# Optimization experiments

Measured on AMD Instinct MI355X. Metric: run time of the kernel, lower is better.

The kernel has to match this reference:

```python
import jax, jax.numpy as jnp
import numpy as np

B, T, D_IN, H = 256, 512, 64, 128
S_MIN, S_FRAC = 0.5, 0.5


def _gru_cell(x_i, h, W_ih, W_hh, b_ih, b_hh):
    # torch.nn.GRUCell semantics
    gi = x_i @ W_ih.T + b_ih          # [B, 3H]
    gh = h @ W_hh.T + b_hh            # [B, 3H]
    i_r, i_z, i_n = jnp.split(gi, 3, axis=-1)
    h_r, h_z, h_n = jnp.split(gh, 3, axis=-1)
    r = jax.nn.sigmoid(i_r + h_r)
    z = jax.nn.sigmoid(i_z + h_z)
    n = jnp.tanh(i_n + r * h_n)
    return (1.0 - z) * n + z * h


def _rk4_step(h, dt, W_node, b_node):
    # one fixed RK4 step of dh/dt = tanh(h @ W_node^T + b_node) over [t, t+dt]
    f = lambda hh: jnp.tanh(hh @ W_node.T + b_node)
    k1 = f(h)
    k2 = f(h + 0.5 * dt * k1)
    k3 = f(h + 0.5 * dt * k2)
    k4 = f(h + dt * k3)
    return h + (dt / 6.0) * (k1 + 2.0 * k2 + 2.0 * k3 + k4)


def setup_inputs() -> dict:
    key = jax.random.key(0)
    ks = jax.random.split(key, 8)
    x = jax.random.normal(ks[0], (B, T, D_IN), dtype=jnp.float32)
    # sorted per-sample time grid; all lens == T so argmax-longest picks row 0
    tp = jnp.broadcast_to(jnp.linspace(0.01, 1.0, T, dtype=jnp.float32), (B, T))
    # generate_samp_mask(x, s_min=0.5, s_frac=0.5), deterministic seed
    rng = np.random.default_rng(0)
    minimum_ind = int(T * S_MIN)
    extrap_ind = int(rng.integers(minimum_ind, T))
    n_inds = int(S_FRAC * extrap_ind)
    samp_inds = np.sort(rng.choice(np.arange(extrap_ind), n_inds, replace=False))
    mask_np = np.zeros(T, dtype=bool)
    mask_np[samp_inds] = True
    samp_mask = jnp.asarray(mask_np)
    s = 1.0 / np.sqrt(H)
    W_ih = jax.random.uniform(ks[1], (3 * H, D_IN), jnp.float32, -s, s)
    W_hh = jax.random.uniform(ks[2], (3 * H, H), jnp.float32, -s, s)
    b_ih = jax.random.uniform(ks[3], (3 * H,), jnp.float32, -s, s)
    b_hh = jax.random.uniform(ks[4], (3 * H,), jnp.float32, -s, s)
    W_node = jax.random.normal(ks[5], (H, H), jnp.float32) * 0.05
    b_node = jnp.zeros((H,), jnp.float32)
    W_out = jax.random.uniform(ks[6], (D_IN, H), jnp.float32, -s, s)
    b_out = jax.random.uniform(ks[7], (D_IN,), jnp.float32, -s, s)
    return {"x": x, "tp": tp, "samp_mask": samp_mask,
            "W_ih": W_ih, "W_hh": W_hh, "b_ih": b_ih, "b_hh": b_hh,
            "W_node": W_node, "b_node": b_node, "W_out": W_out, "b_out": b_out}


def reference(x, tp, samp_mask, W_ih, W_hh, b_ih, b_hh, W_node, b_node, W_out, b_out):
    # get_longest_tp: all lens equal -> row 0; prepend tp[0]-0.01
    t0 = tp[0]                                   # [T]
    ts = jnp.concatenate([t0[:1] - 0.01, t0])    # [T+1]
    dts = ts[1:] - ts[:-1]                       # [T]
    xs = jnp.transpose(x, (1, 0, 2))             # [T, B, D_in]
    h0 = jnp.zeros((x.shape[0], W_hh.shape[1]), x.dtype)

    def step(h, inp):
        dt, x_i, use_x = inp
        h_ode = _rk4_step(h, dt, W_node, b_node)
        prev_out = h @ W_out.T + b_out           # teacher-forcing from own output
        inp_vec = jnp.where(use_x, x_i, prev_out)
        h_new = _gru_cell(inp_vec, h_ode, W_ih, W_hh, b_ih, b_hh)
        return h_new, h_new

    _, h_arr = jax.lax.scan(step, h0, (dts, xs, samp_mask))  # [T, B, H]
    h_arr = jnp.transpose(h_arr, (1, 0, 2))                  # [B, T, H]
    out = h_arr @ W_out.T + b_out                            # [B, T, D_in]
    # select_by_length with all lens == T -> flat [B*T, D_in]
    return out.reshape(-1, out.shape[-1])
```

## Files before the change

### kernel.cpp

```cpp
#include <hip/hip_runtime.h>


#define NB    256
#define TB    512
#define TSTEP 512
#define DIN   64
#define HD    128

typedef float v2f __attribute__((ext_vector_type(2)));

__device__ __forceinline__ float fast_tanh(float v) {
    float e = __expf(2.0f * v);
    return 1.0f - 2.0f / (e + 1.0f);
}
__device__ __forceinline__ float fast_sigmoid(float v) {
    return 1.0f / (1.0f + __expf(-v));
}

__device__ __forceinline__ void sync_lds() {
    asm volatile("s_waitcnt lgkmcnt(0)" ::: "memory");
    __builtin_amdgcn_s_barrier();
    asm volatile("" ::: "memory");
}

template<int PAT>
__device__ __forceinline__ float dpp_xadd(float v) {
    return v + __int_as_float(__builtin_amdgcn_update_dpp(
        0, __float_as_int(v), PAT, 0xF, 0xF, true));
}
template<int OFF>
__device__ __forceinline__ float swz(float v) {
    return __int_as_float(__builtin_amdgcn_ds_swizzle(__float_as_int(v), OFF));
}
__device__ __forceinline__ float red8(float v) {
    v = dpp_xadd<0xB1>(v);
    v = dpp_xadd<0x4E>(v);
    return v + swz<0x101F>(v);
}
__device__ __forceinline__ float red8_split(float pA, float pB, bool low) {
    pA = dpp_xadd<0xB1>(pA);  pB = dpp_xadd<0xB1>(pB);
    pA = dpp_xadd<0x4E>(pA);  pB = dpp_xadd<0x4E>(pB);
    float keep = low ? pA : pB;
    float send = low ? pB : pA;
    return keep + swz<0x101F>(send);
}

__global__ __launch_bounds__(TB, 2) void gruode_kernel(
    const float* __restrict__ x,
    const float* __restrict__ tp,
    const int*   __restrict__ samp_mask,
    const float* __restrict__ W_ih,
    const float* __restrict__ W_hh,
    const float* __restrict__ b_ih,
    const float* __restrict__ b_hh,
    const float* __restrict__ W_node,
    const float* __restrict__ b_node,
    const float* __restrict__ W_out,
    const float* __restrict__ b_out,
    float*       __restrict__ out)
{
    const int t    = threadIdx.x;
    const int b    = blockIdx.x;
    const int jp   = t >> 3;
    const int ks   = t & 7;
    const bool low = (ks & 4) == 0;
    const int jm   = 2 * jp + (ks >> 2);
    const bool own = (ks & 3) == 0;

    __shared__ __align__(16) float sh_h [HD];
    __shared__ __align__(16) float sh_t0[HD];
    __shared__ __align__(16) float sh_t1[HD];
    __shared__ __align__(16) float sh_in[DIN];
    __shared__ __align__(16) float sh_po[DIN];
    __shared__ float sh_dt[TSTEP];
    __shared__ int   sh_mk[TSTEP];

    const float4* Wn4  = (const float4*)W_node;
    const float4* Whh4 = (const float4*)W_hh;
    const float4* Wih4 = (const float4*)W_ih;
    const float4* Wo4  = (const float4*)W_out;

    v2f WnA[8], WnB[8], WhrA[8], WhrB[8], WhzA[8], WhzB[8], WhnA[8], WhnB[8];
    #pragma unroll
    for (int ii = 0; ii < 4; ++ii) {
        float4 w;
        const int c = ii * 8 + ks;
        w = Wn4 [(2*jp  )*32 + c];        WnA [2*ii] = (v2f){w.x,w.y}; WnA [2*ii+1] = (v2f){w.z,w.w};
        w = Wn4 [(2*jp+1)*32 + c];        WnB [2*ii] = (v2f){w.x,w.y}; WnB [2*ii+1] = (v2f){w.z,w.w};
        w = Whh4[(0*HD + 2*jp  )*32 + c]; WhrA[2*ii] = (v2f){w.x,w.y}; WhrA[2*ii+1] = (v2f){w.z,w.w};
        w = Whh4[(0*HD + 2*jp+1)*32 + c]; WhrB[2*ii] = (v2f){w.x,w.y}; WhrB[2*ii+1] = (v2f){w.z,w.w};
        w = Whh4[(1*HD + 2*jp  )*32 + c]; WhzA[2*ii] = (v2f){w.x,w.y}; WhzA[2*ii+1] = (v2f){w.z,w.w};
        w = Whh4[(1*HD + 2*jp+1)*32 + c]; WhzB[2*ii] = (v2f){w.x,w.y}; WhzB[2*ii+1] = (v2f){w.z,w.w};
        w = Whh4[(2*HD + 2*jp  )*32 + c]; WhnA[2*ii] = (v2f){w.x,w.y}; WhnA[2*ii+1] = (v2f){w.z,w.w};
        w = Whh4[(2*HD + 2*jp+1)*32 + c]; WhnB[2*ii] = (v2f){w.x,w.y}; WhnB[2*ii+1] = (v2f){w.z,w.w};
    }
    v2f WirA[4], WirB[4], WizA[4], WizB[4], WinA[4], WinB[4], Wo[8];
    #pragma unroll
    for (int ii = 0; ii < 2; ++ii) {
        float4 w;
        const int c = ii * 8 + ks;
        w = Wih4[(0*HD + 2*jp  )*16 + c]; WirA[2*ii] = (v2f){w.x,w.y}; WirA[2*ii+1] = (v2f){w.z,w.w};
        w = Wih4[(0*HD + 2*jp+1)*16 + c]; WirB[2*ii] = (v2f){w.x,w.y}; WirB[2*ii+1] = (v2f){w.z,w.w};
        w = Wih4[(1*HD + 2*jp  )*16 + c]; WizA[2*ii] = (v2f){w.x,w.y}; WizA[2*ii+1] = (v2f){w.z,w.w};
        w = Wih4[(1*HD + 2*jp+1)*16 + c]; WizB[2*ii] = (v2f){w.x,w.y}; WizB[2*ii+1] = (v2f){w.z,w.w};
        w = Wih4[(2*HD + 2*jp  )*16 + c]; WinA[2*ii] = (v2f){w.x,w.y}; WinA[2*ii+1] = (v2f){w.z,w.w};
        w = Wih4[(2*HD + 2*jp+1)*16 + c]; WinB[2*ii] = (v2f){w.x,w.y}; WinB[2*ii+1] = (v2f){w.z,w.w};
    }
    #pragma unroll
    for (int ii = 0; ii < 4; ++ii) {
        float4 w = Wo4[jp*32 + ii*8 + ks];
        Wo[2*ii] = (v2f){w.x,w.y}; Wo[2*ii+1] = (v2f){w.z,w.w};
    }
    #pragma unroll
    for (int ii = 0; ii < 8; ++ii) {
        asm volatile("" : "+v"(WnA[ii]));  asm volatile("" : "+v"(WnB[ii]));
        asm volatile("" : "+v"(WhrA[ii])); asm volatile("" : "+v"(WhrB[ii]));
        asm volatile("" : "+v"(WhzA[ii])); asm volatile("" : "+v"(WhzB[ii]));
        asm volatile("" : "+v"(WhnA[ii])); asm volatile("" : "+v"(WhnB[ii]));
        asm volatile("" : "+v"(Wo[ii]));
    }
    #pragma unroll
    for (int ii = 0; ii < 4; ++ii) {
        asm volatile("" : "+v"(WirA[ii])); asm volatile("" : "+v"(WirB[ii]));
        asm volatile("" : "+v"(WizA[ii])); asm volatile("" : "+v"(WizB[ii]));
        asm volatile("" : "+v"(WinA[ii])); asm volatile("" : "+v"(WinB[ii]));
    }

    const float bn_s = b_node[jm];
    const float br_s = b_ih[0*HD + jm] + b_hh[0*HD + jm];
    const float bz_s = b_ih[1*HD + jm] + b_hh[1*HD + jm];
    const float bi_s = b_ih[2*HD + jm];
    const float bh_s = b_hh[2*HD + jm];
    const float bo   = b_out[jp];

    if (t < HD) sh_h[t] = 0.0f;
    {
        float tc = tp[t];
        float tq = (t == 0) ? tc - 0.01f : tp[t - 1];
        sh_dt[t] = tc - tq;
        sh_mk[t] = samp_mask[t];
    }

    const float* xbase = x   + (size_t)b * TSTEP * DIN;
    float*       obase = out + (size_t)b * TSTEP * DIN;
    float xr = (t < DIN) ? xbase[t] : 0.0f;

    sync_lds();

    const float4* h4  = (const float4*)sh_h;
    const float4* t04 = (const float4*)sh_t0;
    const float4* t14 = (const float4*)sh_t1;
    const float4* in4 = (const float4*)sh_in;

    auto dot2 = [&](const v2f (&wA)[8], const v2f (&wB)[8], const float4* buf,
                    float& rA, float& rB) {
        v2f aA = {0.f,0.f}, bA = {0.f,0.f}, aB = {0.f,0.f}, bB = {0.f,0.f};
        #pragma unroll
        for (int ii = 0; ii < 4; ++ii) {
            float4 v = buf[ii*8 + ks];
            v2f lo = {v.x, v.y}, hi = {v.z, v.w};
            aA += wA[2*ii] * lo;  bA += wA[2*ii+1] * hi;
            aB += wB[2*ii] * lo;  bB += wB[2*ii+1] * hi;
        }
        v2f sA = aA + bA, sB = aB + bB;
        rA = sA.x + sA.y;  rB = sB.x + sB.y;
    };

    float hj = 0.0f;

    #pragma unroll 1
    for (int s = 0; s < TSTEP; ++s) {
        const float dt = sh_dt[s];
        const int   mc = sh_mk[s];
        float k1, k2, k3;

        {
            float4 v0 = h4[ks], v1 = h4[8+ks], v2 = h4[16+ks], v3 = h4[24+ks];
            v2f l0 = {v0.x,v0.y}, u0 = {v0.z,v0.w};
            v2f l1 = {v1.x,v1.y}, u1 = {v1.z,v1.w};
            v2f l2 = {v2.x,v2.y}, u2 = {v2.z,v2.w};
            v2f l3 = {v3.x,v3.y}, u3 = {v3.z,v3.w};
            v2f aA = WnA[0]*l0 + WnA[1]*u0 + WnA[2]*l1 + WnA[3]*u1
                   + WnA[4]*l2 + WnA[5]*u2 + WnA[6]*l3 + WnA[7]*u3;
            v2f aB = WnB[0]*l0 + WnB[1]*u0 + WnB[2]*l1 + WnB[3]*u1
                   + WnB[4]*l2 + WnB[5]*u2 + WnB[6]*l3 + WnB[7]*u3;
            v2f ao = Wo[0]*l0 + Wo[1]*u0 + Wo[2]*l1 + Wo[3]*u1
                   + Wo[4]*l2 + Wo[5]*u2 + Wo[6]*l3 + Wo[7]*u3;
            k1 = fast_tanh(red8_split(aA.x + aA.y, aB.x + aB.y, low) + bn_s);
            float o = red8(ao.x + ao.y) + bo;
            if (ks == 0) {
                sh_po[jp] = o;
                if (s > 0) obase[(size_t)(s - 1) * DIN + jp] = o;
            }
            if (own) sh_t0[jm] = fmaf(0.5f * dt, k1, hj);
        }
        sync_lds();

        if (t < DIN) sh_in[t] = mc ? xr : sh_po[t];
        {
            float rA, rB;
            dot2(WnA, WnB, t04, rA, rB);
            k2 = fast_tanh(red8_split(rA, rB, low) + bn_s);
            if (own) sh_t1[jm] = fmaf(0.5f * dt, k2, hj);
        }
        {
            const int sn = (s + 1 < TSTEP) ? s + 1 : s;
            if (t < DIN) xr = xbase[(size_t)sn * DIN + t];
        }
        sync_lds();

        float crA, crB, czA, czB, cnA, cnB;
        {
            float rA, rB;
            dot2(WnA, WnB, t14, rA, rB);
            k3 = fast_tanh(red8_split(rA, rB, low) + bn_s);

            float4 v0 = in4[ks], v1 = in4[8 + ks];
            v2f lo0 = {v0.x,v0.y}, hi0 = {v0.z,v0.w};
            v2f lo1 = {v1.x,v1.y}, hi1 = {v1.z,v1.w};
            v2f cr0 = WirA[0]*lo0 + WirA[1]*hi0 + WirA[2]*lo1 + WirA[3]*hi1;
            v2f cr1 = WirB[0]*lo0 + WirB[1]*hi0 + WirB[2]*lo1 + WirB[3]*hi1;
            v2f cz0 = WizA[0]*lo0 + WizA[1]*hi0 + WizA[2]*lo1 + WizA[3]*hi1;
            v2f cz1 = WizB[0]*lo0 + WizB[1]*hi0 + WizB[2]*lo1 + WizB[3]*hi1;
            v2f cn0 = WinA[0]*lo0 + WinA[1]*hi0 + WinA[2]*lo1 + WinA[3]*hi1;
            v2f cn1 = WinB[0]*lo0 + WinB[1]*hi0 + WinB[2]*lo1 + WinB[3]*hi1;
            crA = cr0.x + cr0.y;  crB = cr1.x + cr1.y;
            czA = cz0.x + cz0.y;  czB = cz1.x + cz1.y;
            cnA = cn0.x + cn0.y;  cnB = cn1.x + cn1.y;

            if (own) sh_t0[jm] = fmaf(dt, k3, hj);
        }
        sync_lds();

        float hode = 0.0f;
        {
            float rA, rB;
            dot2(WnA, WnB, t04, rA, rB);
            float k4 = fast_tanh(red8_split(rA, rB, low) + bn_s);
            hode = fmaf(dt * (1.0f / 6.0f),
                        (k1 + 2.0f * k2) + (2.0f * k3 + k4), hj);
            if (own) sh_t1[jm] = hode;
        }
        sync_lds();

        {
            float4 v0 = t14[ks], v1 = t14[8+ks], v2 = t14[16+ks], v3 = t14[24+ks];
            v2f l0 = {v0.x,v0.y}, u0 = {v0.z,v0.w};
            v2f l1 = {v1.x,v1.y}, u1 = {v1.z,v1.w};
            v2f l2 = {v2.x,v2.y}, u2 = {v2.z,v2.w};
            v2f l3 = {v3.x,v3.y}, u3 = {v3.z,v3.w};
            v2f arA = WhrA[0]*l0 + WhrA[1]*u0 + WhrA[2]*l1 + WhrA[3]*u1
                    + WhrA[4]*l2 + WhrA[5]*u2 + WhrA[6]*l3 + WhrA[7]*u3;
            v2f arB = WhrB[0]*l0 + WhrB[1]*u0 + WhrB[2]*l1 + WhrB[3]*u1
                    + WhrB[4]*l2 + WhrB[5]*u2 + WhrB[6]*l3 + WhrB[7]*u3;
            v2f azA = WhzA[0]*l0 + WhzA[1]*u0 + WhzA[2]*l1 + WhzA[3]*u1
                    + WhzA[4]*l2 + WhzA[5]*u2 + WhzA[6]*l3 + WhzA[7]*u3;
            v2f azB = WhzB[0]*l0 + WhzB[1]*u0 + WhzB[2]*l1 + WhzB[3]*u1
                    + WhzB[4]*l2 + WhzB[5]*u2 + WhzB[6]*l3 + WhzB[7]*u3;
            v2f anA = WhnA[0]*l0 + WhnA[1]*u0 + WhnA[2]*l1 + WhnA[3]*u1
                    + WhnA[4]*l2 + WhnA[5]*u2 + WhnA[6]*l3 + WhnA[7]*u3;
            v2f anB = WhnB[0]*l0 + WhnB[1]*u0 + WhnB[2]*l1 + WhnB[3]*u1
                    + WhnB[4]*l2 + WhnB[5]*u2 + WhnB[6]*l3 + WhnB[7]*u3;

            float r_ = red8_split((arA.x + arA.y) + crA, (arB.x + arB.y) + crB, low);
            float z_ = red8_split((azA.x + azA.y) + czA, (azB.x + azB.y) + czB, low);
            float hn = red8_split(anA.x + anA.y, anB.x + anB.y, low);
            float in_ = red8_split(cnA, cnB, low);

            float rr = fast_sigmoid(r_ + br_s);
            float zz = fast_sigmoid(z_ + bz_s);
            float nn = fast_tanh(fmaf(rr, hn + bh_s, in_ + bi_s));
            float hnew = fmaf(zz, hode - nn, nn);
            hj = hnew;
            if (own) sh_h[jm] = hnew;
        }
        sync_lds();
    }

    {
        float4 v0 = h4[ks], v1 = h4[8+ks], v2 = h4[16+ks], v3 = h4[24+ks];
        v2f l0 = {v0.x,v0.y}, u0 = {v0.z,v0.w};
        v2f l1 = {v1.x,v1.y}, u1 = {v1.z,v1.w};
        v2f l2 = {v2.x,v2.y}, u2 = {v2.z,v2.w};
        v2f l3 = {v3.x,v3.y}, u3 = {v3.z,v3.w};
        v2f ao = Wo[0]*l0 + Wo[1]*u0 + Wo[2]*l1 + Wo[3]*u1
               + Wo[4]*l2 + Wo[5]*u2 + Wo[6]*l3 + Wo[7]*u3;
        float o = red8(ao.x + ao.y) + bo;
        if (ks == 0) obase[(size_t)(TSTEP - 1) * DIN + jp] = o;
    }
}

extern "C" void kernel_launch(void* const* d_in, const int* in_sizes, int n_in,
                              void* d_out, int out_size, void* d_ws, size_t ws_size,
                              hipStream_t stream) {
    (void)in_sizes; (void)n_in; (void)d_ws; (void)ws_size; (void)out_size;
    const float* x      = (const float*)d_in[0];
    const float* tp     = (const float*)d_in[1];
    const int*   mask   = (const int*)  d_in[2];
    const float* W_ih   = (const float*)d_in[3];
    const float* W_hh   = (const float*)d_in[4];
    const float* b_ih   = (const float*)d_in[5];
    const float* b_hh   = (const float*)d_in[6];
    const float* W_node = (const float*)d_in[7];
    const float* b_node = (const float*)d_in[8];
    const float* W_out  = (const float*)d_in[9];
    const float* b_out  = (const float*)d_in[10];
    float* outp = (float*)d_out;

    gruode_kernel<<<NB, TB, 0, stream>>>(x, tp, mask, W_ih, W_hh, b_ih, b_hh,
                                         W_node, b_node, W_out, b_out, outp);
}
```

Baseline: 1.099 ms.

## Remap threads to 16-lane groups of four rows with DPP row reductions

Threads are regrouped from 8 lanes covering two output rows into 16 lanes covering four rows, so each lane reads half as many float4 values from shared memory per matvec. The cross-lane reduction now uses only DPP moves (quad add, row_shr, row_bcast-style patterns) in place of ds_swizzle. This is meant to cut LDS read traffic and reduction latency on the serial per-step critical path. In exchange each lane holds four rows of weights, which changes the register layout, and it relies on the DPP patterns having correct semantics within 16-lane rows.

```diff
diff --git a/kernel.cpp b/kernel.cpp
--- a/kernel.cpp
+++ b/kernel.cpp
@@ -28,21 +28,37 @@
     return v + __int_as_float(__builtin_amdgcn_update_dpp(
         0, __float_as_int(v), PAT, 0xF, 0xF, true));
 }
-template<int OFF>
-__device__ __forceinline__ float swz(float v) {
-    return __int_as_float(__builtin_amdgcn_ds_swizzle(__float_as_int(v), OFF));
-}
-__device__ __forceinline__ float red8(float v) {
+template<int PAT>
+__device__ __forceinline__ float dpp_mov(float v) {
+    return __int_as_float(__builtin_amdgcn_update_dpp(
+        0, __float_as_int(v), PAT, 0xF, 0xF, true));
+}
+__device__ __forceinline__ float qred(float v) {
     v = dpp_xadd<0xB1>(v);
-    v = dpp_xadd<0x4E>(v);
-    return v + swz<0x101F>(v);
-}
-__device__ __forceinline__ float red8_split(float pA, float pB, bool low) {
-    pA = dpp_xadd<0xB1>(pA);  pB = dpp_xadd<0xB1>(pB);
-    pA = dpp_xadd<0x4E>(pA);  pB = dpp_xadd<0x4E>(pB);
-    float keep = low ? pA : pB;
-    float send = low ? pB : pA;
-    return keep + swz<0x101F>(send);
+    return dpp_xadd<0x4E>(v);
+}
+__device__ __forceinline__ float red16x4(float p0, float p1, float p2, float p3,
+                                         bool b2, bool b3) {
+    p0 = qred(p0); p1 = qred(p1); p2 = qred(p2); p3 = qred(p3);
+    float u  = b2 ? p2 : p0;
+    float us = b2 ? p0 : p2;
+    float v  = b2 ? p3 : p1;
+    float vs = b2 ? p1 : p3;
+    u += dpp_mov<0x141>(us);
+    v += dpp_mov<0x141>(vs);
+    float w  = b3 ? v : u;
+    float ws = b3 ? u : v;
+    w += dpp_mov<0x128>(ws);
+    return w;
+}
+__device__ __forceinline__ float red16x2(float p0, float p1, bool b3) {
+    p0 = qred(p0); p1 = qred(p1);
+    p0 += dpp_mov<0x141>(p0);
+    p1 += dpp_mov<0x141>(p1);
+    float w  = b3 ? p1 : p0;
+    float ws = b3 ? p0 : p1;
+    w += dpp_mov<0x128>(ws);
+    return w;
 }
 
 __global__ __launch_bounds__(TB, 2) void gruode_kernel(
@@ -61,11 +77,14 @@
 {
     const int t    = threadIdx.x;
     const int b    = blockIdx.x;
-    const int jp   = t >> 3;
-    const int ks   = t & 7;
-    const bool low = (ks & 4) == 0;
-    const int jm   = 2 * jp + (ks >> 2);
-    const bool own = (ks & 3) == 0;
+    const int g    = t >> 4;
+    const int ks2  = t & 15;
+    const bool b2  = (ks2 & 4)  != 0;
+    const bool b3  = (ks2 & 8)  != 0;
+    const int jm   = 4*g + (b2 ? 2 : 0) + (b3 ? 1 : 0);
+    const bool own = (ks2 & 3) == 0;
+    const int jo   = 2*g + (b3 ? 1 : 0);
+    const bool oown= (ks2 & 7) == 0;
 
     __shared__ __align__(16) float sh_h [HD];
     __shared__ __align__(16) float sh_t0[HD];
@@ -80,50 +99,47 @@
     const float4* Wih4 = (const float4*)W_ih;
     const float4* Wo4  = (const float4*)W_out;
 
-    v2f WnA[8], WnB[8], WhrA[8], WhrB[8], WhzA[8], WhzB[8], WhnA[8], WhnB[8];
-    #pragma unroll
-    for (int ii = 0; ii < 4; ++ii) {
-        float4 w;
-        const int c = ii * 8 + ks;
-        w = Wn4 [(2*jp  )*32 + c];        WnA [2*ii] = (v2f){w.x,w.y}; WnA [2*ii+1] = (v2f){w.z,w.w};
-        w = Wn4 [(2*jp+1)*32 + c];        WnB [2*ii] = (v2f){w.x,w.y}; WnB [2*ii+1] = (v2f){w.z,w.w};
-        w = Whh4[(0*HD + 2*jp  )*32 + c]; WhrA[2*ii] = (v2f){w.x,w.y}; WhrA[2*ii+1] = (v2f){w.z,w.w};
-        w = Whh4[(0*HD + 2*jp+1)*32 + c]; WhrB[2*ii] = (v2f){w.x,w.y}; WhrB[2*ii+1] = (v2f){w.z,w.w};
-        w = Whh4[(1*HD + 2*jp  )*32 + c]; WhzA[2*ii] = (v2f){w.x,w.y}; WhzA[2*ii+1] = (v2f){w.z,w.w};
-        w = Whh4[(1*HD + 2*jp+1)*32 + c]; WhzB[2*ii] = (v2f){w.x,w.y}; WhzB[2*ii+1] = (v2f){w.z,w.w};
-        w = Whh4[(2*HD + 2*jp  )*32 + c]; WhnA[2*ii] = (v2f){w.x,w.y}; WhnA[2*ii+1] = (v2f){w.z,w.w};
-        w = Whh4[(2*HD + 2*jp+1)*32 + c]; WhnB[2*ii] = (v2f){w.x,w.y}; WhnB[2*ii+1] = (v2f){w.z,w.w};
-    }
-    v2f WirA[4], WirB[4], WizA[4], WizB[4], WinA[4], WinB[4], Wo[8];
-    #pragma unroll
-    for (int ii = 0; ii < 2; ++ii) {
-        float4 w;
-        const int c = ii * 8 + ks;
-        w = Wih4[(0*HD + 2*jp  )*16 + c]; WirA[2*ii] = (v2f){w.x,w.y}; WirA[2*ii+1] = (v2f){w.z,w.w};
-        w = Wih4[(0*HD + 2*jp+1)*16 + c]; WirB[2*ii] = (v2f){w.x,w.y}; WirB[2*ii+1] = (v2f){w.z,w.w};
-        w = Wih4[(1*HD + 2*jp  )*16 + c]; WizA[2*ii] = (v2f){w.x,w.y}; WizA[2*ii+1] = (v2f){w.z,w.w};
-        w = Wih4[(1*HD + 2*jp+1)*16 + c]; WizB[2*ii] = (v2f){w.x,w.y}; WizB[2*ii+1] = (v2f){w.z,w.w};
-        w = Wih4[(2*HD + 2*jp  )*16 + c]; WinA[2*ii] = (v2f){w.x,w.y}; WinA[2*ii+1] = (v2f){w.z,w.w};
-        w = Wih4[(2*HD + 2*jp+1)*16 + c]; WinB[2*ii] = (v2f){w.x,w.y}; WinB[2*ii+1] = (v2f){w.z,w.w};
-    }
-    #pragma unroll
-    for (int ii = 0; ii < 4; ++ii) {
-        float4 w = Wo4[jp*32 + ii*8 + ks];
-        Wo[2*ii] = (v2f){w.x,w.y}; Wo[2*ii+1] = (v2f){w.z,w.w};
-    }
-    #pragma unroll
-    for (int ii = 0; ii < 8; ++ii) {
-        asm volatile("" : "+v"(WnA[ii]));  asm volatile("" : "+v"(WnB[ii]));
-        asm volatile("" : "+v"(WhrA[ii])); asm volatile("" : "+v"(WhrB[ii]));
-        asm volatile("" : "+v"(WhzA[ii])); asm volatile("" : "+v"(WhzB[ii]));
-        asm volatile("" : "+v"(WhnA[ii])); asm volatile("" : "+v"(WhnB[ii]));
-        asm volatile("" : "+v"(Wo[ii]));
-    }
-    #pragma unroll
-    for (int ii = 0; ii < 4; ++ii) {
-        asm volatile("" : "+v"(WirA[ii])); asm volatile("" : "+v"(WirB[ii]));
-        asm volatile("" : "+v"(WizA[ii])); asm volatile("" : "+v"(WizB[ii]));
-        asm volatile("" : "+v"(WinA[ii])); asm volatile("" : "+v"(WinB[ii]));
+    v2f Wn[16], Whr[16], Whz[16], Whn[16];
+    #pragma unroll
+    for (int r = 0; r < 4; ++r) {
+        const int row = 4*g + r;
+        float4 a, c;
+        a = Wn4 [row*32 + ks2];      Wn [4*r+0]=(v2f){a.x,a.y}; Wn [4*r+1]=(v2f){a.z,a.w};
+        c = Wn4 [row*32 + 16 + ks2]; Wn [4*r+2]=(v2f){c.x,c.y}; Wn [4*r+3]=(v2f){c.z,c.w};
+        a = Whh4[(0*HD+row)*32 + ks2];      Whr[4*r+0]=(v2f){a.x,a.y}; Whr[4*r+1]=(v2f){a.z,a.w};
+        c = Whh4[(0*HD+row)*32 + 16 + ks2]; Whr[4*r+2]=(v2f){c.x,c.y}; Whr[4*r+3]=(v2f){c.z,c.w};
+        a = Whh4[(1*HD+row)*32 + ks2];      Whz[4*r+0]=(v2f){a.x,a.y}; Whz[4*r+1]=(v2f){a.z,a.w};
+        c = Whh4[(1*HD+row)*32 + 16 + ks2]; Whz[4*r+2]=(v2f){c.x,c.y}; Whz[4*r+3]=(v2f){c.z,c.w};
+        a = Whh4[(2*HD+row)*32 + ks2];      Whn[4*r+0]=(v2f){a.x,a.y}; Whn[4*r+1]=(v2f){a.z,a.w};
+        c = Whh4[(2*HD+row)*32 + 16 + ks2]; Whn[4*r+2]=(v2f){c.x,c.y}; Whn[4*r+3]=(v2f){c.z,c.w};
+    }
+    v2f Wir[8], Wiz[8], Win[8];
+    #pragma unroll
+    for (int r = 0; r < 4; ++r) {
+        const int row = 4*g + r;
+        float4 a;
+        a = Wih4[(0*HD+row)*16 + ks2]; Wir[2*r]=(v2f){a.x,a.y}; Wir[2*r+1]=(v2f){a.z,a.w};
+        a = Wih4[(1*HD+row)*16 + ks2]; Wiz[2*r]=(v2f){a.x,a.y}; Wiz[2*r+1]=(v2f){a.z,a.w};
+        a = Wih4[(2*HD+row)*16 + ks2]; Win[2*r]=(v2f){a.x,a.y}; Win[2*r+1]=(v2f){a.z,a.w};
+    }
+    v2f Wo[8];
+    #pragma unroll
+    for (int o = 0; o < 2; ++o) {
+        const int row = 2*g + o;
+        float4 a = Wo4[row*32 + ks2];
+        float4 c = Wo4[row*32 + 16 + ks2];
+        Wo[4*o+0]=(v2f){a.x,a.y}; Wo[4*o+1]=(v2f){a.z,a.w};
+        Wo[4*o+2]=(v2f){c.x,c.y}; Wo[4*o+3]=(v2f){c.z,c.w};
+    }
+    #pragma unroll
+    for (int i = 0; i < 16; ++i) {
+        asm volatile("" : "+v"(Wn[i]));  asm volatile("" : "+v"(Whr[i]));
+        asm volatile("" : "+v"(Whz[i])); asm volatile("" : "+v"(Whn[i]));
+    }
+    #pragma unroll
+    for (int i = 0; i < 8; ++i) {
+        asm volatile("" : "+v"(Wir[i])); asm volatile("" : "+v"(Wiz[i]));
+        asm volatile("" : "+v"(Win[i])); asm volatile("" : "+v"(Wo[i]));
     }
 
     const float bn_s = b_node[jm];
@@ -131,7 +147,7 @@
     const float bz_s = b_ih[1*HD + jm] + b_hh[1*HD + jm];
     const float bi_s = b_ih[2*HD + jm];
     const float bh_s = b_hh[2*HD + jm];
-    const float bo   = b_out[jp];
+    const float bo_s = b_out[jo];
 
     if (t < HD) sh_h[t] = 0.0f;
     {
@@ -152,18 +168,18 @@
     const float4* t14 = (const float4*)sh_t1;
     const float4* in4 = (const float4*)sh_in;
 
-    auto dot2 = [&](const v2f (&wA)[8], const v2f (&wB)[8], const float4* buf,
-                    float& rA, float& rB) {
-        v2f aA = {0.f,0.f}, bA = {0.f,0.f}, aB = {0.f,0.f}, bB = {0.f,0.f};
+    auto lds2 = [&](const float4* buf, v2f& l0, v2f& u0, v2f& l1, v2f& u1) {
+        float4 v0 = buf[ks2], v1 = buf[16 + ks2];
+        l0 = (v2f){v0.x, v0.y}; u0 = (v2f){v0.z, v0.w};
+        l1 = (v2f){v1.x, v1.y}; u1 = (v2f){v1.z, v1.w};
+    };
+    auto dot4 = [&](const v2f (&W)[16], v2f l0, v2f u0, v2f l1, v2f u1,
+                    float (&p)[4]) {
         #pragma unroll
-        for (int ii = 0; ii < 4; ++ii) {
-            float4 v = buf[ii*8 + ks];
-            v2f lo = {v.x, v.y}, hi = {v.z, v.w};
-            aA += wA[2*ii] * lo;  bA += wA[2*ii+1] * hi;
-            aB += wB[2*ii] * lo;  bB += wB[2*ii+1] * hi;
-        }
-        v2f sA = aA + bA, sB = aB + bB;
-        rA = sA.x + sA.y;  rB = sB.x + sB.y;
+        for (int r = 0; r < 4; ++r) {
+            v2f a = W[4*r]*l0 + W[4*r+1]*u0 + W[4*r+2]*l1 + W[4*r+3]*u1;
+            p[r] = a.x + a.y;
+        }
     };
 
     float hj = 0.0f;
@@ -175,22 +191,15 @@
         float k1, k2, k3;
 
         {
-            float4 v0 = h4[ks], v1 = h4[8+ks], v2 = h4[16+ks], v3 = h4[24+ks];
-            v2f l0 = {v0.x,v0.y}, u0 = {v0.z,v0.w};
-            v2f l1 = {v1.x,v1.y}, u1 = {v1.z,v1.w};
-            v2f l2 = {v2.x,v2.y}, u2 = {v2.z,v2.w};
-            v2f l3 = {v3.x,v3.y}, u3 = {v3.z,v3.w};
-            v2f aA = WnA[0]*l0 + WnA[1]*u0 + WnA[2]*l1 + WnA[3]*u1
-                   + WnA[4]*l2 + WnA[5]*u2 + WnA[6]*l3 + WnA[7]*u3;
-            v2f aB = WnB[0]*l0 + WnB[1]*u0 + WnB[2]*l1 + WnB[3]*u1
-                   + WnB[4]*l2 + WnB[5]*u2 + WnB[6]*l3 + WnB[7]*u3;
-            v2f ao = Wo[0]*l0 + Wo[1]*u0 + Wo[2]*l1 + Wo[3]*u1
-                   + Wo[4]*l2 + Wo[5]*u2 + Wo[6]*l3 + Wo[7]*u3;
-            k1 = fast_tanh(red8_split(aA.x + aA.y, aB.x + aB.y, low) + bn_s);
-            float o = red8(ao.x + ao.y) + bo;
-            if (ks == 0) {
-                sh_po[jp] = o;
-                if (s > 0) obase[(size_t)(s - 1) * DIN + jp] = o;
+            v2f l0,u0,l1,u1; lds2(h4, l0,u0,l1,u1);
+            float p[4]; dot4(Wn, l0,u0,l1,u1, p);
+            v2f ao0 = Wo[0]*l0 + Wo[1]*u0 + Wo[2]*l1 + Wo[3]*u1;
+            v2f ao1 = Wo[4]*l0 + Wo[5]*u0 + Wo[6]*l1 + Wo[7]*u1;
+            k1 = fast_tanh(red16x4(p[0],p[1],p[2],p[3], b2,b3) + bn_s);
+            float o = red16x2(ao0.x + ao0.y, ao1.x + ao1.y, b3) + bo_s;
+            if (oown) {
+                sh_po[jo] = o;
+                if (s > 0) obase[(size_t)(s - 1) * DIN + jo] = o;
             }
             if (own) sh_t0[jm] = fmaf(0.5f * dt, k1, hj);
         }
@@ -198,9 +207,9 @@
 
         if (t < DIN) sh_in[t] = mc ? xr : sh_po[t];
         {
-            float rA, rB;
-            dot2(WnA, WnB, t04, rA, rB);
-            k2 = fast_tanh(red8_split(rA, rB, low) + bn_s);
+            v2f l0,u0,l1,u1; lds2(t04, l0,u0,l1,u1);
+            float p[4]; dot4(Wn, l0,u0,l1,u1, p);
+            k2 = fast_tanh(red16x4(p[0],p[1],p[2],p[3], b2,b3) + bn_s);
             if (own) sh_t1[jm] = fmaf(0.5f * dt, k2, hj);
         }
         {
@@ -209,34 +218,30 @@
         }
         sync_lds();
 
-        float crA, crB, czA, czB, cnA, cnB;
-        {
-            float rA, rB;
-            dot2(WnA, WnB, t14, rA, rB);
-            k3 = fast_tanh(red8_split(rA, rB, low) + bn_s);
-
-            float4 v0 = in4[ks], v1 = in4[8 + ks];
-            v2f lo0 = {v0.x,v0.y}, hi0 = {v0.z,v0.w};
-            v2f lo1 = {v1.x,v1.y}, hi1 = {v1.z,v1.w};
-            v2f cr0 = WirA[0]*lo0 + WirA[1]*hi0 + WirA[2]*lo1 + WirA[3]*hi1;
-            v2f cr1 = WirB[0]*lo0 + WirB[1]*hi0 + WirB[2]*lo1 + WirB[3]*hi1;
-            v2f cz0 = WizA[0]*lo0 + WizA[1]*hi0 + WizA[2]*lo1 + WizA[3]*hi1;
-            v2f cz1 = WizB[0]*lo0 + WizB[1]*hi0 + WizB[2]*lo1 + WizB[3]*hi1;
-            v2f cn0 = WinA[0]*lo0 + WinA[1]*hi0 + WinA[2]*lo1 + WinA[3]*hi1;
-            v2f cn1 = WinB[0]*lo0 + WinB[1]*hi0 + WinB[2]*lo1 + WinB[3]*hi1;
-            crA = cr0.x + cr0.y;  crB = cr1.x + cr1.y;
-            czA = cz0.x + cz0.y;  czB = cz1.x + cz1.y;
-            cnA = cn0.x + cn0.y;  cnB = cn1.x + cn1.y;
-
+        float cr[4], cz[4], cn[4];
+        {
+            v2f l0,u0,l1,u1; lds2(t14, l0,u0,l1,u1);
+            float p[4]; dot4(Wn, l0,u0,l1,u1, p);
+            k3 = fast_tanh(red16x4(p[0],p[1],p[2],p[3], b2,b3) + bn_s);
+
+            float4 vi = in4[ks2];
+            v2f li = (v2f){vi.x, vi.y}, ui = (v2f){vi.z, vi.w};
+            #pragma unroll
+            for (int r = 0; r < 4; ++r) {
+                v2f a = Wir[2*r]*li + Wir[2*r+1]*ui;
+                v2f c = Wiz[2*r]*li + Wiz[2*r+1]*ui;
+                v2f d = Win[2*r]*li + Win[2*r+1]*ui;
+                cr[r] = a.x + a.y;  cz[r] = c.x + c.y;  cn[r] = d.x + d.y;
+            }
             if (own) sh_t0[jm] = fmaf(dt, k3, hj);
         }
         sync_lds();
 
-        float hode = 0.0f;
-        {
-            float rA, rB;
-            dot2(WnA, WnB, t04, rA, rB);
-            float k4 = fast_tanh(red8_split(rA, rB, low) + bn_s);
+        float hode;
+        {
+            v2f l0,u0,l1,u1; lds2(t04, l0,u0,l1,u1);
+            float p[4]; dot4(Wn, l0,u0,l1,u1, p);
+            float k4 = fast_tanh(red16x4(p[0],p[1],p[2],p[3], b2,b3) + bn_s);
             hode = fmaf(dt * (1.0f / 6.0f),
                         (k1 + 2.0f * k2) + (2.0f * k3 + k4), hj);
             if (own) sh_t1[jm] = hode;
@@ -244,32 +249,19 @@
         sync_lds();
 
         {
-            float4 v0 = t14[ks], v1 = t14[8+ks], v2 = t14[16+ks], v3 = t14[24+ks];
-            v2f l0 = {v0.x,v0.y}, u0 = {v0.z,v0.w};
-            v2f l1 = {v1.x,v1.y}, u1 = {v1.z,v1.w};
-            v2f l2 = {v2.x,v2.y}, u2 = {v2.z,v2.w};
-            v2f l3 = {v3.x,v3.y}, u3 = {v3.z,v3.w};
-            v2f arA = WhrA[0]*l0 + WhrA[1]*u0 + WhrA[2]*l1 + WhrA[3]*u1
-                    + WhrA[4]*l2 + WhrA[5]*u2 + WhrA[6]*l3 + WhrA[7]*u3;
-            v2f arB = WhrB[0]*l0 + WhrB[1]*u0 + WhrB[2]*l1 + WhrB[3]*u1
-                    + WhrB[4]*l2 + WhrB[5]*u2 + WhrB[6]*l3 + WhrB[7]*u3;
-            v2f azA = WhzA[0]*l0 + WhzA[1]*u0 + WhzA[2]*l1 + WhzA[3]*u1
-                    + WhzA[4]*l2 + WhzA[5]*u2 + WhzA[6]*l3 + WhzA[7]*u3;
-            v2f azB = WhzB[0]*l0 + WhzB[1]*u0 + WhzB[2]*l1 + WhzB[3]*u1
-                    + WhzB[4]*l2 + WhzB[5]*u2 + WhzB[6]*l3 + WhzB[7]*u3;
-            v2f anA = WhnA[0]*l0 + WhnA[1]*u0 + WhnA[2]*l1 + WhnA[3]*u1
-                    + WhnA[4]*l2 + WhnA[5]*u2 + WhnA[6]*l3 + WhnA[7]*u3;
-            v2f anB = WhnB[0]*l0 + WhnB[1]*u0 + WhnB[2]*l1 + WhnB[3]*u1
-                    + WhnB[4]*l2 + WhnB[5]*u2 + WhnB[6]*l3 + WhnB[7]*u3;
-
-            float r_ = red8_split((arA.x + arA.y) + crA, (arB.x + arB.y) + crB, low);
-            float z_ = red8_split((azA.x + azA.y) + czA, (azB.x + azB.y) + czB, low);
-            float hn = red8_split(anA.x + anA.y, anB.x + anB.y, low);
-            float in_ = red8_split(cnA, cnB, low);
+            v2f l0,u0,l1,u1; lds2(t14, l0,u0,l1,u1);
+            float ar[4], az[4], an[4];
+            dot4(Whr, l0,u0,l1,u1, ar);
+            dot4(Whz, l0,u0,l1,u1, az);
+            dot4(Whn, l0,u0,l1,u1, an);
+            float r_  = red16x4(ar[0]+cr[0], ar[1]+cr[1], ar[2]+cr[2], ar[3]+cr[3], b2,b3);
+            float z_  = red16x4(az[0]+cz[0], az[1]+cz[1], az[2]+cz[2], az[3]+cz[3], b2,b3);
+            float hn  = red16x4(an[0], an[1], an[2], an[3], b2,b3);
+            float cns = red16x4(cn[0], cn[1], cn[2], cn[3], b2,b3);
 
             float rr = fast_sigmoid(r_ + br_s);
             float zz = fast_sigmoid(z_ + bz_s);
-            float nn = fast_tanh(fmaf(rr, hn + bh_s, in_ + bi_s));
+            float nn = fast_tanh(fmaf(rr, hn + bh_s, cns + bi_s));
             float hnew = fmaf(zz, hode - nn, nn);
             hj = hnew;
             if (own) sh_h[jm] = hnew;
@@ -278,15 +270,11 @@
     }
 
     {
-        float4 v0 = h4[ks], v1 = h4[8+ks], v2 = h4[16+ks], v3 = h4[24+ks];
-        v2f l0 = {v0.x,v0.y}, u0 = {v0.z,v0.w};
-        v2f l1 = {v1.x,v1.y}, u1 = {v1.z,v1.w};
-        v2f l2 = {v2.x,v2.y}, u2 = {v2.z,v2.w};
-        v2f l3 = {v3.x,v3.y}, u3 = {v3.z,v3.w};
-        v2f ao = Wo[0]*l0 + Wo[1]*u0 + Wo[2]*l1 + Wo[3]*u1
-               + Wo[4]*l2 + Wo[5]*u2 + Wo[6]*l3 + Wo[7]*u3;
-        float o = red8(ao.x + ao.y) + bo;
-        if (ks == 0) obase[(size_t)(TSTEP - 1) * DIN + jp] = o;
+        v2f l0,u0,l1,u1; lds2(h4, l0,u0,l1,u1);
+        v2f ao0 = Wo[0]*l0 + Wo[1]*u0 + Wo[2]*l1 + Wo[3]*u1;
+        v2f ao1 = Wo[4]*l0 + Wo[5]*u0 + Wo[6]*l1 + Wo[7]*u1;
+        float o = red16x2(ao0.x + ao0.y, ao1.x + ao1.y, b3) + bo_s;
+        if (oown) obase[(size_t)(TSTEP - 1) * DIN + jo] = o;
     }
 }
 
```

After: 1.354 ms. 1.23x slower.
